# Optimization experiments

Measured on AMD Instinct MI355X. Metric: run time of the kernel, lower is better.

The kernel has to match this reference:

```python
import jax, jax.numpy as jnp
import numpy as np

N_NODES = 100000
N_EDGES = 1600000
D = 64


def _sage_conv(x, src, dst, W_l, W_r, b):
    # PyG SAGEConv (aggr='mean'): out_i = W_l @ mean_{j in N(i)} x_j + W_r @ x_i + b
    n = x.shape[0]
    msgs = x[src]  # [E, D] gather of source-node features
    agg = jax.ops.segment_sum(msgs, dst, num_segments=n)  # [N, D]
    cnt = jax.ops.segment_sum(jnp.ones((src.shape[0],), x.dtype), dst, num_segments=n)
    mean = agg / jnp.maximum(cnt, 1.0)[:, None]
    return mean @ W_l.T + x @ W_r.T + b


def setup_inputs() -> dict:
    key = jax.random.key(0)
    ks = jax.random.split(key, 8)
    s = 1.0 / np.sqrt(D)
    x = jax.random.normal(ks[0], (N_NODES, D), dtype=jnp.float32)
    edge_index = jax.random.randint(ks[1], (2, N_EDGES), 0, N_NODES, dtype=jnp.int64)
    return {
        "x": x,
        "edge_index": edge_index,
        "W1_l": jax.random.normal(ks[2], (D, D), dtype=jnp.float32) * s,
        "W1_r": jax.random.normal(ks[3], (D, D), dtype=jnp.float32) * s,
        "b1": jnp.zeros((D,), dtype=jnp.float32),
        "W2_l": jax.random.normal(ks[4], (D, D), dtype=jnp.float32) * s,
        "W2_r": jax.random.normal(ks[5], (D, D), dtype=jnp.float32) * s,
        "b2": jnp.zeros((D,), dtype=jnp.float32),
    }


def reference(x, edge_index, W1_l, W1_r, b1, W2_l, W2_r, b2):
    src, dst = edge_index[0], edge_index[1]
    h = _sage_conv(x, src, dst, W1_l, W1_r, b1)
    h = jax.nn.relu(h)
    out = _sage_conv(h, src, dst, W2_l, W2_r, b2)
    return out
```

## Files before the change

### kernel.cpp

```cpp
#include <hip/hip_runtime.h>

#define D 64
#define BSH2 6
#define BN2 (1 << BSH2)
#define NBK_MAX 2048
#define CAP2SH 11
#define CAP2 (1 << CAP2SH)
#define SIDX_MAX (CAP2 + 3 * BN2)

typedef __attribute__((ext_vector_type(8))) short bf16x8;
typedef __attribute__((ext_vector_type(4))) float f32x4;

__device__ __forceinline__ unsigned int f2bf_rne(float f) {
    unsigned int b = __float_as_uint(f);
    return (b + 0x7fffu + ((b >> 16) & 1u)) >> 16;
}
__device__ __forceinline__ unsigned int pack_bf(float lo, float hi) {
    return f2bf_rne(lo) | (f2bf_rne(hi) << 16);
}
__device__ __forceinline__ float bflo(unsigned int u) { return __uint_as_float(u << 16); }
__device__ __forceinline__ float bfhi(unsigned int u) { return __uint_as_float(u & 0xffff0000u); }

__global__ void cast_kernel(const float4* __restrict__ xin, uint2* __restrict__ xb, int n4,
                            int* __restrict__ cnt, int nz) {
    int gid = blockIdx.x * blockDim.x + threadIdx.x;
    if (gid < nz) cnt[gid] = 0;
    int stride = gridDim.x * blockDim.x;
    for (int i = gid; i < n4; i += stride) {
        float4 v = xin[i];
        uint2 o;
        o.x = pack_bf(v.x, v.y);
        o.y = pack_bf(v.z, v.w);
        xb[i] = o;
    }
}

__global__ __launch_bounds__(256) void binscatter_kernel(
    const int* __restrict__ src, const int* __restrict__ dst,
    int* __restrict__ cnt, unsigned int* __restrict__ pairs,
    int E, int NBK, int CE) {
    __shared__ int lh[NBK_MAX];
    __shared__ int lbase[NBK_MAX];
    for (int k = threadIdx.x; k < NBK; k += 256) lh[k] = 0;
    __syncthreads();
    int b = blockIdx.x;
    int beg = b * CE, end = min(beg + CE, E);
    for (int e = beg + threadIdx.x; e < end; e += 256)
        atomicAdd(&lh[dst[e] >> BSH2], 1);
    __syncthreads();
    for (int k = threadIdx.x; k < NBK; k += 256) {
        int c = lh[k];
        if (c) lbase[k] = (k << CAP2SH) + atomicAdd(&cnt[k], c);
        lh[k] = 0;
    }
    __syncthreads();
    for (int e = beg + threadIdx.x; e < end; e += 256) {
        int d = dst[e];
        int k = d >> BSH2;
        int r = atomicAdd(&lh[k], 1);
        pairs[lbase[k] + r] = (unsigned int)src[e] | ((unsigned int)(d & (BN2 - 1)) << 17);
    }
}

__global__ __launch_bounds__(256) void fused_layer_kernel(
    const unsigned int* __restrict__ xin, const unsigned int* __restrict__ pairs,
    const int* __restrict__ cnt,
    const float* __restrict__ Wl, const float* __restrict__ Wr,
    const float* __restrict__ bias,
    float* __restrict__ outf, unsigned int* __restrict__ outb, int N, int relu) {
    __shared__ uint4 smean[BN2][8];
    __shared__ int sidx[SIDX_MAX];
    __shared__ int lcnt[BN2];
    __shared__ int lbase[BN2];
    __shared__ int lcur[BN2];
    __shared__ int sscan[BN2];

    unsigned int* spr = (unsigned int*)&smean[0][0];

    int tid = threadIdx.x;
    int wave = tid >> 6;
    int lane = tid & 63;
    int b = blockIdx.x;
    int node0 = b << BSH2;

    int cntk = min(cnt[b], CAP2);
    if (tid < BN2) lcnt[tid] = 0;
    __syncthreads();
    int rbeg = b << CAP2SH;
    for (int i = tid; i < cntk; i += 256) {
        unsigned int rec = pairs[rbeg + i];
        spr[i] = rec;
        atomicAdd(&lcnt[rec >> 17], 1);
    }
    __syncthreads();
    int deg = (tid < BN2) ? lcnt[tid] : 0;
    int ps  = (deg + 3) & ~3;
    if (tid < BN2) sscan[tid] = ps;
    __syncthreads();
    for (int off = 1; off < BN2; off <<= 1) {
        int t = (tid < BN2 && tid >= off) ? sscan[tid - off] : 0;
        __syncthreads();
        if (tid < BN2) sscan[tid] += t;
        __syncthreads();
    }
    if (tid < BN2) {
        int base = sscan[tid] - ps;
        lbase[tid] = base;
        lcur[tid] = base;
    }
    __syncthreads();
    for (int i = tid; i < cntk; i += 256) {
        unsigned int rec = spr[i];
        int j = rec >> 17;
        int pos = atomicAdd(&lcur[j], 1);
        sidx[pos] = (int)(rec & 0x1FFFFu);
    }
    __syncthreads();

    int q  = lane >> 3;
    int fl = lane & 7;
    for (int o = 0; o < 2; ++o) {
        int nl = (wave << 4) + (o << 3) + q;
        int beg = lbase[nl];
        int dg  = lcnt[nl];
        int end = beg + dg;
        float s0 = 0.f, s1 = 0.f, s2 = 0.f, s3 = 0.f;
        float s4 = 0.f, s5 = 0.f, s6 = 0.f, s7 = 0.f;
        int j = beg;
        for (; j + 4 <= end; j += 4) {
            int4 iv = *(const int4*)(sidx + j);
            uint4 u0 = *(const uint4*)(xin + iv.x * 32 + fl * 4);
            uint4 u1 = *(const uint4*)(xin + iv.y * 32 + fl * 4);
            uint4 u2 = *(const uint4*)(xin + iv.z * 32 + fl * 4);
            uint4 u3 = *(const uint4*)(xin + iv.w * 32 + fl * 4);
            s0 += bflo(u0.x) + bflo(u1.x) + bflo(u2.x) + bflo(u3.x);
            s1 += bfhi(u0.x) + bfhi(u1.x) + bfhi(u2.x) + bfhi(u3.x);
            s2 += bflo(u0.y) + bflo(u1.y) + bflo(u2.y) + bflo(u3.y);
            s3 += bfhi(u0.y) + bfhi(u1.y) + bfhi(u2.y) + bfhi(u3.y);
            s4 += bflo(u0.z) + bflo(u1.z) + bflo(u2.z) + bflo(u3.z);
            s5 += bfhi(u0.z) + bfhi(u1.z) + bfhi(u2.z) + bfhi(u3.z);
            s6 += bflo(u0.w) + bflo(u1.w) + bflo(u2.w) + bflo(u3.w);
            s7 += bfhi(u0.w) + bfhi(u1.w) + bfhi(u2.w) + bfhi(u3.w);
        }
        for (; j < end; ++j) {
            uint4 u = *(const uint4*)(xin + sidx[j] * 32 + fl * 4);
            s0 += bflo(u.x); s1 += bfhi(u.x);
            s2 += bflo(u.y); s3 += bfhi(u.y);
            s4 += bflo(u.z); s5 += bfhi(u.z);
            s6 += bflo(u.w); s7 += bfhi(u.w);
        }
        float inv = 1.0f / fmaxf((float)dg, 1.0f);
        uint4 ov;
        ov.x = pack_bf(s0 * inv, s1 * inv);
        ov.y = pack_bf(s2 * inv, s3 * inv);
        ov.z = pack_bf(s4 * inv, s5 * inv);
        ov.w = pack_bf(s6 * inv, s7 * inv);
        smean[nl][fl ^ (nl & 7)] = ov;
    }

    int lm   = lane & 15;
    int quad = lane >> 4;
    int f_a  = (wave << 4) + lm;
    bf16x8 wh[4], wlo[4];
#pragma unroll
    for (int s = 0; s < 4; ++s) {
        int k8 = s * 32 + quad * 8;
        const float* Wsrc = (k8 < 64) ? Wl : Wr;
        const float* p = Wsrc + f_a * 64 + (k8 & 63);
        float4 w0 = *(const float4*)p;
        float4 w1 = *(const float4*)(p + 4);
        float w[8] = {w0.x, w0.y, w0.z, w0.w, w1.x, w1.y, w1.z, w1.w};
        bf16x8 h, l;
#pragma unroll
        for (int jj = 0; jj < 8; ++jj) {
            unsigned int hb = f2bf_rne(w[jj]);
            float hf = __uint_as_float(hb << 16);
            unsigned int lb = f2bf_rne(w[jj] - hf);
            h[jj] = (short)hb;
            l[jj] = (short)lb;
        }
        wh[s] = h;
        wlo[s] = l;
    }

    __syncthreads();

    f32x4 acc[4];
#pragma unroll
    for (int nt = 0; nt < 4; ++nt) acc[nt] = (f32x4){0.f, 0.f, 0.f, 0.f};

#pragma unroll
    for (int nt = 0; nt < 4; ++nt) {
        int nl = nt * 16 + lm;
        int node = node0 + nl;
        bool v = node < N;
        const unsigned int* xrow = xin + (long long)node * 32;
#pragma unroll
        for (int s = 0; s < 2; ++s) {
            union { uint4 u4; bf16x8 v8; } cv;
            cv.u4 = smean[nl][(s * 4 + quad) ^ (lm & 7)];
            acc[nt] = __builtin_amdgcn_mfma_f32_16x16x32_bf16(wh[s],  cv.v8, acc[nt], 0, 0, 0);
            acc[nt] = __builtin_amdgcn_mfma_f32_16x16x32_bf16(wlo[s], cv.v8, acc[nt], 0, 0, 0);
        }
#pragma unroll
        for (int s = 2; s < 4; ++s) {
            uint4 u = make_uint4(0u, 0u, 0u, 0u);
            if (v) u = *(const uint4*)(xrow + ((s & 1) << 4) + (quad << 2));
            union { uint4 u4; bf16x8 v8; } cv;
            cv.u4 = u;
            acc[nt] = __builtin_amdgcn_mfma_f32_16x16x32_bf16(wh[s],  cv.v8, acc[nt], 0, 0, 0);
            acc[nt] = __builtin_amdgcn_mfma_f32_16x16x32_bf16(wlo[s], cv.v8, acc[nt], 0, 0, 0);
        }
    }

    int fb = (wave << 4) + quad * 4;
    float4 bv = *(const float4*)(bias + fb);
#pragma unroll
    for (int nt = 0; nt < 4; ++nt) {
        int node = node0 + nt * 16 + lm;
        if (node >= N) continue;
        float r0 = acc[nt][0] + bv.x;
        float r1 = acc[nt][1] + bv.y;
        float r2 = acc[nt][2] + bv.z;
        float r3 = acc[nt][3] + bv.w;
        if (relu) {
            r0 = fmaxf(r0, 0.f); r1 = fmaxf(r1, 0.f);
            r2 = fmaxf(r2, 0.f); r3 = fmaxf(r3, 0.f);
        }
        if (outf) *(float4*)(outf + (long long)node * D + fb) = make_float4(r0, r1, r2, r3);
        if (outb) *(uint2*)(outb + (long long)node * 32 + (fb >> 1)) =
                      make_uint2(pack_bf(r0, r1), pack_bf(r2, r3));
    }
}

extern "C" void kernel_launch(void* const* d_in, const int* in_sizes, int n_in,
                              void* d_out, int out_size, void* d_ws, size_t ws_size,
                              hipStream_t stream) {
    const float* x   = (const float*)d_in[0];
    const int* ei    = (const int*)d_in[1];
    const float* W1l = (const float*)d_in[2];
    const float* W1r = (const float*)d_in[3];
    const float* b1  = (const float*)d_in[4];
    const float* W2l = (const float*)d_in[5];
    const float* W2r = (const float*)d_in[6];
    const float* b2  = (const float*)d_in[7];

    const int E = in_sizes[1] / 2;
    const int N = in_sizes[0] / D;
    const int* src  = ei;
    const int* dstp = ei + E;
    const int NBK = (N + BN2 - 1) >> BSH2;
    const int G1 = 512;
    const int CE = (E + G1 - 1) / G1;

    char* ws = (char*)d_ws;
    size_t off = 0;
    auto alloc = [&](size_t bytes) { void* p = ws + off; off = (off + bytes + 255) & ~(size_t)255; return p; };
    int* cnt            = (int*)alloc((size_t)NBK * 4);
    unsigned int* pairs = (unsigned int*)alloc(((size_t)(NBK + 1) << CAP2SH) * 4);
    unsigned int* xb    = (unsigned int*)alloc((size_t)N * 32 * 4);
    unsigned int* hb    = (unsigned int*)alloc((size_t)N * 32 * 4);

    float* out = (float*)d_out;

    cast_kernel<<<2048, 256, 0, stream>>>((const float4*)x, (uint2*)xb, N * 16, cnt, NBK);

    binscatter_kernel<<<G1, 256, 0, stream>>>(src, dstp, cnt, pairs, E, NBK, CE);

    fused_layer_kernel<<<NBK, 256, 0, stream>>>(xb, pairs, cnt, W1l, W1r, b1,
                                                nullptr, hb, N, 1);
    fused_layer_kernel<<<NBK, 256, 0, stream>>>(hb, pairs, cnt, W2l, W2r, b2,
                                                out, nullptr, N, 0);
}
```

Baseline: 221.1 us.

## Bin edges into coarse 512-node regions and filter per sub-block in layer kernel

Binscatter now buckets edges by 512-node region (196 bins) instead of 64-node blocks (1563 bins), which cuts global atomics and scattered writes per block and makes pair writes more contiguous. Each layer block then scans its whole region's pair list and keeps only records for its 64-node sub-block, with a block-index swizzle that spreads regions across the grid. The cost is that every region's pairs are read eight times per layer, plus an extra shared atomic per kept record.

```diff
diff --git a/kernel.cpp b/kernel.cpp
--- a/kernel.cpp
+++ b/kernel.cpp
@@ -3,10 +3,13 @@
 #define D 64
 #define BSH2 6
 #define BN2 (1 << BSH2)
-#define NBK_MAX 2048
-#define CAP2SH 11
-#define CAP2 (1 << CAP2SH)
-#define SIDX_MAX (CAP2 + 3 * BN2)
+#define RSH 9
+#define RN (1 << RSH)
+#define NR_MAX 256
+#define RCAPSH 14
+#define RCAP (1 << RCAPSH)
+#define SPR_MAX 2048
+#define SIDX_MAX (SPR_MAX + 3 * BN2)
 
 typedef __attribute__((ext_vector_type(8))) short bf16x8;
 typedef __attribute__((ext_vector_type(4))) float f32x4;
@@ -38,27 +41,27 @@
 __global__ __launch_bounds__(256) void binscatter_kernel(
     const int* __restrict__ src, const int* __restrict__ dst,
     int* __restrict__ cnt, unsigned int* __restrict__ pairs,
-    int E, int NBK, int CE) {
-    __shared__ int lh[NBK_MAX];
-    __shared__ int lbase[NBK_MAX];
-    for (int k = threadIdx.x; k < NBK; k += 256) lh[k] = 0;
+    int E, int NR, int CE) {
+    __shared__ int lh[NR_MAX];
+    __shared__ int lbase[NR_MAX];
+    for (int k = threadIdx.x; k < NR; k += 256) lh[k] = 0;
     __syncthreads();
     int b = blockIdx.x;
     int beg = b * CE, end = min(beg + CE, E);
     for (int e = beg + threadIdx.x; e < end; e += 256)
-        atomicAdd(&lh[dst[e] >> BSH2], 1);
-    __syncthreads();
-    for (int k = threadIdx.x; k < NBK; k += 256) {
+        atomicAdd(&lh[dst[e] >> RSH], 1);
+    __syncthreads();
+    for (int k = threadIdx.x; k < NR; k += 256) {
         int c = lh[k];
-        if (c) lbase[k] = (k << CAP2SH) + atomicAdd(&cnt[k], c);
+        if (c) lbase[k] = (k << RCAPSH) + atomicAdd(&cnt[k], c);
         lh[k] = 0;
     }
     __syncthreads();
     for (int e = beg + threadIdx.x; e < end; e += 256) {
         int d = dst[e];
-        int k = d >> BSH2;
+        int k = d >> RSH;
         int r = atomicAdd(&lh[k], 1);
-        pairs[lbase[k] + r] = (unsigned int)src[e] | ((unsigned int)(d & (BN2 - 1)) << 17);
+        pairs[lbase[k] + r] = (unsigned int)src[e] | ((unsigned int)(d & (RN - 1)) << 17);
     }
 }
 
@@ -67,32 +70,47 @@
     const int* __restrict__ cnt,
     const float* __restrict__ Wl, const float* __restrict__ Wr,
     const float* __restrict__ bias,
-    float* __restrict__ outf, unsigned int* __restrict__ outb, int N, int relu) {
+    float* __restrict__ outf, unsigned int* __restrict__ outb,
+    int N, int NR, int relu) {
     __shared__ uint4 smean[BN2][8];
     __shared__ int sidx[SIDX_MAX];
     __shared__ int lcnt[BN2];
     __shared__ int lbase[BN2];
     __shared__ int lcur[BN2];
     __shared__ int sscan[BN2];
+    __shared__ int scnt0;
 
     unsigned int* spr = (unsigned int*)&smean[0][0];
+
+    int x = blockIdx.x & 7;
+    int j = blockIdx.x >> 3;
+    int region = ((j >> 3) << 3) | x;
+    int sub = j & 7;
+    if (region >= NR) return;
+    int node0 = (region << RSH) + (sub << BSH2);
+    if (node0 >= N) return;
 
     int tid = threadIdx.x;
     int wave = tid >> 6;
     int lane = tid & 63;
-    int b = blockIdx.x;
-    int node0 = b << BSH2;
-
-    int cntk = min(cnt[b], CAP2);
+
+    if (tid == 0) scnt0 = 0;
     if (tid < BN2) lcnt[tid] = 0;
     __syncthreads();
-    int rbeg = b << CAP2SH;
-    for (int i = tid; i < cntk; i += 256) {
-        unsigned int rec = pairs[rbeg + i];
-        spr[i] = rec;
-        atomicAdd(&lcnt[rec >> 17], 1);
-    }
-    __syncthreads();
+    int cR = min(cnt[region], RCAP);
+    int rb = region << RCAPSH;
+    for (int i = tid; i < cR; i += 256) {
+        unsigned int rec = pairs[rb + i];
+        if (((rec >> 23) & 7u) == (unsigned int)sub) {
+            int p = atomicAdd(&scnt0, 1);
+            if (p < SPR_MAX) {
+                spr[p] = rec;
+                atomicAdd(&lcnt[(rec >> 17) & (BN2 - 1)], 1);
+            }
+        }
+    }
+    __syncthreads();
+    int cntk = min(scnt0, SPR_MAX);
     int deg = (tid < BN2) ? lcnt[tid] : 0;
     int ps  = (deg + 3) & ~3;
     if (tid < BN2) sscan[tid] = ps;
@@ -111,8 +129,8 @@
     __syncthreads();
     for (int i = tid; i < cntk; i += 256) {
         unsigned int rec = spr[i];
-        int j = rec >> 17;
-        int pos = atomicAdd(&lcur[j], 1);
+        int jn = (rec >> 17) & (BN2 - 1);
+        int pos = atomicAdd(&lcur[jn], 1);
         sidx[pos] = (int)(rec & 0x1FFFFu);
     }
     __syncthreads();
@@ -126,9 +144,9 @@
         int end = beg + dg;
         float s0 = 0.f, s1 = 0.f, s2 = 0.f, s3 = 0.f;
         float s4 = 0.f, s5 = 0.f, s6 = 0.f, s7 = 0.f;
-        int j = beg;
-        for (; j + 4 <= end; j += 4) {
-            int4 iv = *(const int4*)(sidx + j);
+        int jj = beg;
+        for (; jj + 4 <= end; jj += 4) {
+            int4 iv = *(const int4*)(sidx + jj);
             uint4 u0 = *(const uint4*)(xin + iv.x * 32 + fl * 4);
             uint4 u1 = *(const uint4*)(xin + iv.y * 32 + fl * 4);
             uint4 u2 = *(const uint4*)(xin + iv.z * 32 + fl * 4);
@@ -142,8 +160,8 @@
             s6 += bflo(u0.w) + bflo(u1.w) + bflo(u2.w) + bflo(u3.w);
             s7 += bfhi(u0.w) + bfhi(u1.w) + bfhi(u2.w) + bfhi(u3.w);
         }
-        for (; j < end; ++j) {
-            uint4 u = *(const uint4*)(xin + sidx[j] * 32 + fl * 4);
+        for (; jj < end; ++jj) {
+            uint4 u = *(const uint4*)(xin + sidx[jj] * 32 + fl * 4);
             s0 += bflo(u.x); s1 += bfhi(u.x);
             s2 += bflo(u.y); s3 += bfhi(u.y);
             s4 += bflo(u.z); s5 += bfhi(u.z);
@@ -249,26 +267,27 @@
     const int N = in_sizes[0] / D;
     const int* src  = ei;
     const int* dstp = ei + E;
-    const int NBK = (N + BN2 - 1) >> BSH2;
+    const int NR = (N + RN - 1) >> RSH;
     const int G1 = 512;
     const int CE = (E + G1 - 1) / G1;
+    const int G2 = 64 * ((NR + 7) >> 3);
 
     char* ws = (char*)d_ws;
     size_t off = 0;
     auto alloc = [&](size_t bytes) { void* p = ws + off; off = (off + bytes + 255) & ~(size_t)255; return p; };
-    int* cnt            = (int*)alloc((size_t)NBK * 4);
-    unsigned int* pairs = (unsigned int*)alloc(((size_t)(NBK + 1) << CAP2SH) * 4);
+    int* cnt            = (int*)alloc((size_t)NR * 4);
+    unsigned int* pairs = (unsigned int*)alloc(((size_t)(NR + 1) << RCAPSH) * 4);
     unsigned int* xb    = (unsigned int*)alloc((size_t)N * 32 * 4);
     unsigned int* hb    = (unsigned int*)alloc((size_t)N * 32 * 4);
 
     float* out = (float*)d_out;
 
-    cast_kernel<<<2048, 256, 0, stream>>>((const float4*)x, (uint2*)xb, N * 16, cnt, NBK);
-
-    binscatter_kernel<<<G1, 256, 0, stream>>>(src, dstp, cnt, pairs, E, NBK, CE);
-
-    fused_layer_kernel<<<NBK, 256, 0, stream>>>(xb, pairs, cnt, W1l, W1r, b1,
-                                                nullptr, hb, N, 1);
-    fused_layer_kernel<<<NBK, 256, 0, stream>>>(hb, pairs, cnt, W2l, W2r, b2,
-                                                out, nullptr, N, 0);
-}
+    cast_kernel<<<2048, 256, 0, stream>>>((const float4*)x, (uint2*)xb, N * 16, cnt, NR);
+
+    binscatter_kernel<<<G1, 256, 0, stream>>>(src, dstp, cnt, pairs, E, NR, CE);
+
+    fused_layer_kernel<<<G2, 256, 0, stream>>>(xb, pairs, cnt, W1l, W1r, b1,
+                                               nullptr, hb, N, NR, 1);
+    fused_layer_kernel<<<G2, 256, 0, stream>>>(hb, pairs, cnt, W2l, W2r, b2,
+                                               out, nullptr, N, NR, 0);
+}
```

Result: slower. 251.6 us (+13.8%).
